# Kernel optimization log

Measured on AMD Instinct MI355X. Metric: run time of the kernel, lower is better.

## Reference

```python
import jax, jax.numpy as jnp
import numpy as np

VOCAB = 50000
EMB = 200        # embedding_size
CAP = 3          # capitalization_size
IN = EMB + CAP   # LSTM input size = 203
HID = 128        # LSTMCell(128)
B = 256
T = 500          # comment_length
NC = 6           # num_classes
DENSE = 64


def _lstm_scan(x_tbi, W, b):
    """x_tbi: [T,B,IN]. W: [IN+HID, 4*HID] (tf gate order i, j, f, o), b: [4*HID].
    Returns h sequence [T,B,HID]. forget_bias=1.0 as in tf.contrib.rnn.LSTMCell."""
    h0 = jnp.zeros((x_tbi.shape[1], HID), x_tbi.dtype)

    def step(carry, x):
        h, c = carry
        gates = jnp.concatenate([x, h], axis=-1) @ W + b   # [B, 4*HID]
        i, j, f, o = jnp.split(gates, 4, axis=-1)
        c = jax.nn.sigmoid(f + 1.0) * c + jax.nn.sigmoid(i) * jnp.tanh(j)
        h = jax.nn.sigmoid(o) * jnp.tanh(c)
        return (h, c), h

    _, hs = jax.lax.scan(step, (h0, h0), x_tbi)
    return hs


def setup_inputs() -> dict:
    key = jax.random.key(0)
    ks = jax.random.split(key, 12)
    words = jax.random.randint(ks[0], (B, T), 0, VOCAB, dtype=jnp.int32)
    capitals = jax.random.randint(ks[1], (B, T), 0, CAP, dtype=jnp.int32)
    # word embeddings: random trainable table with a trailing zero-padding row
    word_emb = jax.random.normal(ks[2], (VOCAB + 1, EMB), dtype=jnp.float32) * 0.1
    # capitalization embedding: one_hot_embedding_matrix(3) = [eye(3); zeros(1,3)]
    cap_emb = jnp.concatenate([jnp.eye(CAP, dtype=jnp.float32),
                               jnp.zeros((1, CAP), dtype=jnp.float32)], axis=0)
    def glorot(k, shape):
        lim = np.sqrt(6.0 / (shape[0] + shape[1]))
        return jax.random.uniform(k, shape, jnp.float32, -lim, lim)
    W_fw = glorot(ks[3], (IN + HID, 4 * HID))
    b_fw = jnp.zeros((4 * HID,), jnp.float32)
    W_bw = glorot(ks[4], (IN + HID, 4 * HID))
    b_bw = jnp.zeros((4 * HID,), jnp.float32)
    W1 = glorot(ks[5], (2 * HID, DENSE))
    b1 = jnp.zeros((DENSE,), jnp.float32)
    W2 = glorot(ks[6], (DENSE, NC))
    b2 = jnp.zeros((NC,), jnp.float32)
    return {"words": words, "capitals": capitals, "word_emb": word_emb,
            "cap_emb": cap_emb, "W_fw": W_fw, "b_fw": b_fw,
            "W_bw": W_bw, "b_bw": b_bw, "W1": W1, "b1": b1,
            "W2": W2, "b2": b2}


def reference(words, capitals, word_emb, cap_emb, W_fw, b_fw, W_bw, b_bw,
              W1, b1, W2, b2):
    # embedding lookups and concat -> [B, T, 203]
    x = jnp.concatenate([word_emb[words], cap_emb[capitals]], axis=-1)
    x_tbi = jnp.transpose(x, (1, 0, 2))                    # [T, B, IN]
    # forward direction: take output at last timestep
    h_fw_last = _lstm_scan(x_tbi, W_fw, b_fw)[-1]          # [B, HID]
    # backward direction: bidirectional_dynamic_rnn reverses bw outputs back,
    # so outputs[1][:, 0, :] == last state of scan over the reversed sequence
    h_bw_first = _lstm_scan(x_tbi[::-1], W_bw, b_bw)[-1]   # [B, HID]
    rnn_output = jnp.concatenate([h_fw_last, h_bw_first], axis=1)  # [B, 256]
    dense1 = jax.nn.elu(rnn_output @ W1 + b1)              # [B, 64]
    y_hat = jax.nn.sigmoid(dense1 @ W2 + b2)               # [B, NC]
    return y_hat
```

## Files before the change

### kernel.cpp

```cpp
#include <hip/hip_runtime.h>

#define T 500
#define NB 256
#define VROWS 50001
#define EMB 200
#define KPAD 224
#define MPAD 50048

typedef unsigned short u16;
typedef __attribute__((ext_vector_type(8))) __bf16 bf16x8;
typedef __attribute__((ext_vector_type(8))) short short8;
typedef __attribute__((ext_vector_type(4))) float f32x4;
typedef __attribute__((ext_vector_type(4))) u16 u16x4;
typedef __attribute__((ext_vector_type(4))) int i32x4;

__device__ __forceinline__ u16 f2bf(float x) {
  union { float f; unsigned u; } v; v.f = x;
  unsigned r = (v.u + 0x7fffu + ((v.u >> 16) & 1u)) >> 16;
  return (u16)r;
}
__device__ __forceinline__ float bf2f(u16 b) {
  union { unsigned u; float f; } v; v.u = ((unsigned)b) << 16;
  return v.f;
}
__device__ __forceinline__ float rcp_(float x) { return __builtin_amdgcn_rcpf(x); }
__device__ __forceinline__ float sig_(float x) { return rcp_(1.f + __expf(-x)); }
__device__ __forceinline__ float tanh_(float x) { return 1.f - 2.f * rcp_(1.f + __expf(2.f * x)); }

__global__ void prep_kernel(const int* __restrict__ words, const int* __restrict__ caps,
                            const float* __restrict__ word_emb,
                            const float* __restrict__ cap_emb,
                            const float* __restrict__ Wfw, const float* __restrict__ bfw,
                            const float* __restrict__ Wbw, const float* __restrict__ bbw,
                            int* __restrict__ wordsT, int* __restrict__ capsT,
                            float* __restrict__ Cproj, u16* __restrict__ Apad,
                            u16* __restrict__ Bt) {
  const int S0 = NB * T;
  const int S1 = MPAD * (KPAD / 4);
  const int S2 = 2 * 512 * KPAD;
  const int S3 = 2 * 4 * 512;
  int tid = blockIdx.x * blockDim.x + threadIdx.x;
  int nthr = gridDim.x * blockDim.x;
  for (int i = tid; i < S0 + S1 + S2 + S3; i += nthr) {
    if (i < S0) {
      int b = i / T, t = i - b * T;
      wordsT[t * NB + b] = words[i];
      capsT[t * NB + b]  = caps[i];
    } else if (i < S0 + S1) {
      int idx = i - S0;
      int v = idx / (KPAD / 4), q = idx - v * (KPAD / 4);
      int k = q * 4;
      u16x4 o;
      if (v < VROWS && k < EMB) {
        const float* p = word_emb + (size_t)v * EMB + k;
        o[0] = f2bf(p[0]); o[1] = f2bf(p[1]); o[2] = f2bf(p[2]); o[3] = f2bf(p[3]);
      } else {
        o[0] = o[1] = o[2] = o[3] = 0;
      }
      *(u16x4*)(Apad + (size_t)v * KPAD + k) = o;
    } else if (i < S0 + S1 + S2) {
      int idx = i - S0 - S1;
      int d = idx / (512 * KPAD), rem = idx - d * (512 * KPAD);
      int colp = rem / KPAD, k = rem - colp * KPAD;
      const float* W = d ? Wbw : Wfw;
      int g = colp & 3, jj = colp >> 2;
      Bt[idx] = (k < EMB) ? f2bf(W[k * 512 + g * 128 + jj]) : (u16)0;
    } else {
      int idx = i - S0 - S1 - S2;
      int dir = idx >> 11; int c = (idx >> 9) & 3; int colp = idx & 511;
      int j = colp >> 2, g = colp & 3;
      const float* W = dir ? Wbw : Wfw;
      const float* bias = dir ? bbw : bfw;
      float v = bias[g * 128 + j];
      #pragma unroll
      for (int cc = 0; cc < 3; ++cc)
        v += cap_emb[c * 3 + cc] * W[(200 + cc) * 512 + g * 128 + j];
      Cproj[idx] = v;
    }
  }
}

__global__ __launch_bounds__(256) void vproj_kernel(
    const u16* __restrict__ Apad, const u16* __restrict__ Bt,
    u16* __restrict__ Vfw, u16* __restrict__ Vbw) {
  const int mt = blockIdx.x, nt = blockIdx.y, dir = blockIdx.z;
  const u16* __restrict__ B = Bt + (size_t)dir * 512 * KPAD;
  u16* __restrict__ V = dir ? Vbw : Vfw;

  __shared__ u16 Al[2][128 * 32];
  __shared__ u16 Bl[2][128 * 32];

  const int tid = threadIdx.x;
  const int w = tid >> 6, l = tid & 63;
  const int la = l & 15, lb = l >> 4;
  const int m0 = mt * 128, n0 = nt * 128;

  auto stage = [&](int buf, int ks) {
    int k0 = ks * 32;
    #pragma unroll
    for (int h = 0; h < 2; ++h) {
      int c = w * 128 + h * 64 + l;
      int row = c >> 2, kq = c & 3;
      const u16* ga = Apad + (size_t)(m0 + row) * KPAD + k0 + kq * 8;
      __builtin_amdgcn_global_load_lds(
          (const __attribute__((address_space(1))) void*)ga,
          (__attribute__((address_space(3))) void*)&Al[buf][(w * 128 + h * 64) * 8],
          16, 0, 0);
      const u16* gb = B + (size_t)(n0 + row) * KPAD + k0 + kq * 8;
      __builtin_amdgcn_global_load_lds(
          (const __attribute__((address_space(1))) void*)gb,
          (__attribute__((address_space(3))) void*)&Bl[buf][(w * 128 + h * 64) * 8],
          16, 0, 0);
    }
  };

  f32x4 z = {0.f, 0.f, 0.f, 0.f};
  f32x4 acc[4][4] = {{z,z,z,z},{z,z,z,z},{z,z,z,z},{z,z,z,z}};
  const int wr = w >> 1, wc = w & 1;

  stage(0, 0);
  __syncthreads();
  #pragma unroll 1
  for (int ks = 0; ks < 7; ++ks) {
    int cur = ks & 1;
    if (ks < 6) stage(cur ^ 1, ks + 1);
    bf16x8 af[4], bfr[4];
    #pragma unroll
    for (int m = 0; m < 4; ++m)
      af[m] = *(const bf16x8*)&Al[cur][(wr * 64 + m * 16 + la) * 32 + lb * 8];
    #pragma unroll
    for (int n = 0; n < 4; ++n)
      bfr[n] = *(const bf16x8*)&Bl[cur][(wc * 64 + n * 16 + la) * 32 + lb * 8];
    #pragma unroll
    for (int m = 0; m < 4; ++m)
      #pragma unroll
      for (int n = 0; n < 4; ++n)
        acc[m][n] = __builtin_amdgcn_mfma_f32_16x16x32_bf16(af[m], bfr[n], acc[m][n], 0, 0, 0);
    __syncthreads();
  }

  #pragma unroll
  for (int m = 0; m < 4; ++m) {
    #pragma unroll
    for (int n = 0; n < 4; ++n) {
      #pragma unroll
      for (int r = 0; r < 4; ++r) {
        int v = m0 + wr * 64 + m * 16 + lb * 4 + r;
        int colp = n0 + wc * 64 + n * 16 + la;
        V[(size_t)v * 512 + colp] = f2bf(acc[m][n][r]);
      }
    }
  }
}

template <int P>
__device__ __forceinline__ void lstm_step(
    int t, int dir, int b0, int la, int lb, int j,
    const int* __restrict__ wordsT, const int* __restrict__ capsT,
    const u16* __restrict__ V, const float* __restrict__ Cp,
    const bf16x8 (&bfrag)[4][4], u16 (&hbuf)[2][16][136],
    u16x4 (&vw)[4], f32x4 (&cp)[4],
    i32x4& wio, i32x4& cio, u16x4 (&vwo)[4], f32x4 (&cpo)[4],
    i32x4& wis, i32x4& cis, f32x4& cst, f32x4& hl) {
  {
    int ts = t + 2; if (ts > T - 1) ts = T - 1;
    int tt = dir ? (T - 1 - ts) : ts;
    wis = *(const i32x4*)(wordsT + tt * NB + b0 + lb * 4);
    cis = *(const i32x4*)(capsT + tt * NB + b0 + lb * 4);
  }
  #pragma unroll
  for (int r = 0; r < 4; ++r) {
    vwo[r] = *(const u16x4*)(V + (size_t)wio[r] * 512 + j * 4);
    cpo[r] = *(const f32x4*)(Cp + cio[r] * 512 + j * 4);
  }

  bf16x8 afr[4];
  #pragma unroll
  for (int kk = 0; kk < 4; ++kk)
    afr[kk] = *(const bf16x8*)&hbuf[P][la][kk * 32 + lb * 8];

  f32x4 acc0, acc1, acc2, acc3;
  #pragma unroll
  for (int r = 0; r < 4; ++r) {
    acc0[r] = bf2f(vw[r][0]) + cp[r][0];
    acc1[r] = bf2f(vw[r][1]) + cp[r][1];
    acc2[r] = bf2f(vw[r][2]) + cp[r][2];
    acc3[r] = bf2f(vw[r][3]) + cp[r][3];
  }
  #pragma unroll
  for (int kk = 0; kk < 4; ++kk) {
    acc0 = __builtin_amdgcn_mfma_f32_16x16x32_bf16(afr[kk], bfrag[0][kk], acc0, 0, 0, 0);
    acc1 = __builtin_amdgcn_mfma_f32_16x16x32_bf16(afr[kk], bfrag[1][kk], acc1, 0, 0, 0);
    acc2 = __builtin_amdgcn_mfma_f32_16x16x32_bf16(afr[kk], bfrag[2][kk], acc2, 0, 0, 0);
    acc3 = __builtin_amdgcn_mfma_f32_16x16x32_bf16(afr[kk], bfrag[3][kk], acc3, 0, 0, 0);
  }
  #pragma unroll
  for (int r = 0; r < 4; ++r) {
    float fg = sig_(acc2[r] + 1.f);
    float ig = sig_(acc0[r]);
    float tj = tanh_(acc1[r]);
    float cn = fg * cst[r] + ig * tj;
    cst[r] = cn;
    float hn = sig_(acc3[r]) * tanh_(cn);
    hl[r] = hn;
    hbuf[P ^ 1][lb * 4 + r][j] = f2bf(hn);
  }
  asm volatile("s_waitcnt lgkmcnt(0)\n\ts_barrier" ::: "memory");
}

__global__ __launch_bounds__(512, 1) void lstm_kernel(
    const int* __restrict__ wordsT, const int* __restrict__ capsT,
    const u16* __restrict__ Vfw, const u16* __restrict__ Vbw,
    const float* __restrict__ CprojAll, const float* __restrict__ Wfw,
    const float* __restrict__ Wbw, float* __restrict__ rnn) {
  const int dir = blockIdx.x & 1;
  const int chunk = blockIdx.x >> 1;
  const int b0 = chunk * 16;
  const u16* __restrict__ V = dir ? Vbw : Vfw;
  const float* __restrict__ Cp = CprojAll + dir * 4 * 512;
  const float* __restrict__ W = dir ? Wbw : Wfw;

  const int tid = threadIdx.x;
  const int w = tid >> 6, l = tid & 63, la = l & 15, lb = l >> 4;
  const int j = w * 16 + la;

  bf16x8 bfrag[4][4];
  #pragma unroll
  for (int g = 0; g < 4; ++g) {
    #pragma unroll
    for (int kk = 0; kk < 4; ++kk) {
      short8 t8;
      #pragma unroll
      for (int r = 0; r < 8; ++r) {
        int k = kk * 32 + lb * 8 + r;
        t8[r] = (short)f2bf(W[(203 + k) * 512 + g * 128 + j]);
      }
      bfrag[g][kk] = __builtin_bit_cast(bf16x8, t8);
    }
  }

  __shared__ u16 hbuf[2][16][136];
  for (int i = tid; i < 2 * 16 * 136; i += 512) ((u16*)hbuf)[i] = 0;

  f32x4 cst = {0.f, 0.f, 0.f, 0.f};
  f32x4 hl  = {0.f, 0.f, 0.f, 0.f};

  i32x4 wiA, ciA, wiB, ciB;
  u16x4 vwA[4]; f32x4 cpA[4];
  u16x4 vwB[4]; f32x4 cpB[4];
  {
    int tt0 = dir ? (T - 1) : 0;
    wiA = *(const i32x4*)(wordsT + tt0 * NB + b0 + lb * 4);
    ciA = *(const i32x4*)(capsT + tt0 * NB + b0 + lb * 4);
    int tt1 = dir ? (T - 2) : 1;
    wiB = *(const i32x4*)(wordsT + tt1 * NB + b0 + lb * 4);
    ciB = *(const i32x4*)(capsT + tt1 * NB + b0 + lb * 4);
  }
  #pragma unroll
  for (int r = 0; r < 4; ++r) {
    vwA[r] = *(const u16x4*)(V + (size_t)wiA[r] * 512 + j * 4);
    cpA[r] = *(const f32x4*)(Cp + ciA[r] * 512 + j * 4);
  }
  __syncthreads();

  #pragma unroll 1
  for (int tp = 0; tp < T / 2; ++tp) {
    int t0 = 2 * tp;
    lstm_step<0>(t0,     dir, b0, la, lb, j, wordsT, capsT, V, Cp, bfrag, hbuf,
                 vwA, cpA, wiB, ciB, vwB, cpB, wiA, ciA, cst, hl);
    lstm_step<1>(t0 + 1, dir, b0, la, lb, j, wordsT, capsT, V, Cp, bfrag, hbuf,
                 vwB, cpB, wiA, ciA, vwA, cpA, wiB, ciB, cst, hl);
  }

  #pragma unroll
  for (int r = 0; r < 4; ++r)
    rnn[(size_t)(b0 + lb * 4 + r) * 256 + dir * 128 + j] = hl[r];
}

__global__ void head_kernel(const float* __restrict__ rnn, const float* __restrict__ W1,
                            const float* __restrict__ b1, const float* __restrict__ W2,
                            const float* __restrict__ b2, float* __restrict__ out) {
  int b = blockIdx.x;
  int jj = threadIdx.x;
  __shared__ float d1[64];
  float acc = b1[jj];
  const float* r = rnn + b * 256;
  #pragma unroll 4
  for (int k = 0; k < 256; ++k) acc += r[k] * W1[k * 64 + jj];
  d1[jj] = acc > 0.f ? acc : (__expf(acc) - 1.f);
  __syncthreads();
  if (jj < 6) {
    float a2 = b2[jj];
    #pragma unroll 8
    for (int k = 0; k < 64; ++k) a2 += d1[k] * W2[k * 6 + jj];
    out[b * 6 + jj] = rcp_(1.f + __expf(-a2));
  }
}

extern "C" void kernel_launch(void* const* d_in, const int* in_sizes, int n_in,
                              void* d_out, int out_size, void* d_ws, size_t ws_size,
                              hipStream_t stream) {
  (void)in_sizes; (void)n_in; (void)out_size; (void)ws_size;
  const int*   words    = (const int*)  d_in[0];
  const int*   caps     = (const int*)  d_in[1];
  const float* word_emb = (const float*)d_in[2];
  const float* cap_emb  = (const float*)d_in[3];
  const float* Wfw      = (const float*)d_in[4];
  const float* bfw      = (const float*)d_in[5];
  const float* Wbw      = (const float*)d_in[6];
  const float* bbw      = (const float*)d_in[7];
  const float* W1       = (const float*)d_in[8];
  const float* b1       = (const float*)d_in[9];
  const float* W2       = (const float*)d_in[10];
  const float* b2       = (const float*)d_in[11];
  float* out = (float*)d_out;

  char* base = (char*)d_ws;
  size_t off = 0;
  auto alloc = [&](size_t bytes) {
    char* q = base + off;
    off = (off + bytes + 255) & ~(size_t)255;
    return q;
  };
  u16*   Vfw    = (u16*)  alloc((size_t)MPAD * 512 * 2);
  u16*   Vbw    = (u16*)  alloc((size_t)MPAD * 512 * 2);
  u16*   Apad   = (u16*)  alloc((size_t)MPAD * KPAD * 2);
  u16*   Bt     = (u16*)  alloc((size_t)2 * 512 * KPAD * 2);
  int*   wordsT = (int*)  alloc((size_t)T * NB * 4);
  int*   capsT  = (int*)  alloc((size_t)T * NB * 4);
  float* Cproj  = (float*)alloc((size_t)2 * 4 * 512 * 4);
  float* rnn    = (float*)alloc((size_t)256 * 256 * 4);

  hipLaunchKernelGGL(prep_kernel, dim3(2048), dim3(256), 0, stream,
                     words, caps, word_emb, cap_emb, Wfw, bfw, Wbw, bbw,
                     wordsT, capsT, Cproj, Apad, Bt);
  hipLaunchKernelGGL(vproj_kernel, dim3(MPAD / 128, 4, 2), dim3(256), 0, stream,
                     Apad, Bt, Vfw, Vbw);
  hipLaunchKernelGGL(lstm_kernel, dim3(32), dim3(512), 0, stream,
                     wordsT, capsT, Vfw, Vbw, Cproj, Wfw, Wbw, rnn);
  hipLaunchKernelGGL(head_kernel, dim3(256), dim3(64), 0, stream,
                     rnn, W1, b1, W2, b2, out);
}
```

Before: 670.3 us.

## Deepen LSTM gather prefetch to four steps and XOR-swizzle hidden-state LDS

The recurrent loop now prefetches word indices four steps ahead and gathered input projections two steps ahead, using four rotating register sets so global gather latency has more steps to hide behind the serial recurrence. The padded hidden-state shared buffer is replaced by an unpadded buffer with an XOR swizzle to avoid bank conflicts on reads and writes. The float-to-bf16 conversion now uses the native cast. These changes raise register pressure and add more in-flight loads per step.

```diff
diff --git a/kernel.cpp b/kernel.cpp
--- a/kernel.cpp
+++ b/kernel.cpp
@@ -15,9 +15,8 @@
 typedef __attribute__((ext_vector_type(4))) int i32x4;
 
 __device__ __forceinline__ u16 f2bf(float x) {
-  union { float f; unsigned u; } v; v.f = x;
-  unsigned r = (v.u + 0x7fffu + ((v.u >> 16) & 1u)) >> 16;
-  return (u16)r;
+  __bf16 h = (__bf16)x;
+  return __builtin_bit_cast(u16, h);
 }
 __device__ __forceinline__ float bf2f(u16 b) {
   union { unsigned u; float f; } v; v.u = ((unsigned)b) << 16;
@@ -153,39 +152,43 @@
   }
 }
 
-template <int P>
+template <int PAR>
 __device__ __forceinline__ void lstm_step(
     int t, int dir, int b0, int la, int lb, int j,
     const int* __restrict__ wordsT, const int* __restrict__ capsT,
     const u16* __restrict__ V, const float* __restrict__ Cp,
-    const bf16x8 (&bfrag)[4][4], u16 (&hbuf)[2][16][136],
-    u16x4 (&vw)[4], f32x4 (&cp)[4],
-    i32x4& wio, i32x4& cio, u16x4 (&vwo)[4], f32x4 (&cpo)[4],
-    i32x4& wis, i32x4& cis, f32x4& cst, f32x4& hl) {
+    const bf16x8 (&bfrag)[4][4], u16* __restrict__ hbuf,
+    u16x4 (&vw_c)[4], f32x4 (&cp_c)[4],
+    i32x4& wi_c, i32x4& ci_c,
+    i32x4& wi_g, i32x4& ci_g,
+    u16x4 (&vw_g)[4], f32x4 (&cp_g)[4],
+    f32x4& cst, f32x4& hl) {
   {
-    int ts = t + 2; if (ts > T - 1) ts = T - 1;
+    int ts = t + 4; if (ts > T - 1) ts = T - 1;
     int tt = dir ? (T - 1 - ts) : ts;
-    wis = *(const i32x4*)(wordsT + tt * NB + b0 + lb * 4);
-    cis = *(const i32x4*)(capsT + tt * NB + b0 + lb * 4);
+    wi_c = *(const i32x4*)(wordsT + tt * NB + b0 + lb * 4);
+    ci_c = *(const i32x4*)(capsT + tt * NB + b0 + lb * 4);
   }
   #pragma unroll
   for (int r = 0; r < 4; ++r) {
-    vwo[r] = *(const u16x4*)(V + (size_t)wio[r] * 512 + j * 4);
-    cpo[r] = *(const f32x4*)(Cp + cio[r] * 512 + j * 4);
-  }
-
+    vw_g[r] = *(const u16x4*)(V + (size_t)wi_g[r] * 512 + j * 4);
+    cp_g[r] = *(const f32x4*)(Cp + ci_g[r] * 512 + j * 4);
+  }
+
+  const u16* hb = hbuf + PAR * 2048;
+  const int swz = (la & 7) << 3;
   bf16x8 afr[4];
   #pragma unroll
   for (int kk = 0; kk < 4; ++kk)
-    afr[kk] = *(const bf16x8*)&hbuf[P][la][kk * 32 + lb * 8];
+    afr[kk] = *(const bf16x8*)(hb + ((la * 128 + kk * 32 + lb * 8) ^ swz));
 
   f32x4 acc0, acc1, acc2, acc3;
   #pragma unroll
   for (int r = 0; r < 4; ++r) {
-    acc0[r] = bf2f(vw[r][0]) + cp[r][0];
-    acc1[r] = bf2f(vw[r][1]) + cp[r][1];
-    acc2[r] = bf2f(vw[r][2]) + cp[r][2];
-    acc3[r] = bf2f(vw[r][3]) + cp[r][3];
+    acc0[r] = bf2f(vw_c[r][0]) + cp_c[r][0];
+    acc1[r] = bf2f(vw_c[r][1]) + cp_c[r][1];
+    acc2[r] = bf2f(vw_c[r][2]) + cp_c[r][2];
+    acc3[r] = bf2f(vw_c[r][3]) + cp_c[r][3];
   }
   #pragma unroll
   for (int kk = 0; kk < 4; ++kk) {
@@ -194,6 +197,7 @@
     acc2 = __builtin_amdgcn_mfma_f32_16x16x32_bf16(afr[kk], bfrag[2][kk], acc2, 0, 0, 0);
     acc3 = __builtin_amdgcn_mfma_f32_16x16x32_bf16(afr[kk], bfrag[3][kk], acc3, 0, 0, 0);
   }
+  u16* ho = hbuf + (PAR ^ 1) * 2048;
   #pragma unroll
   for (int r = 0; r < 4; ++r) {
     float fg = sig_(acc2[r] + 1.f);
@@ -203,7 +207,8 @@
     cst[r] = cn;
     float hn = sig_(acc3[r]) * tanh_(cn);
     hl[r] = hn;
-    hbuf[P ^ 1][lb * 4 + r][j] = f2bf(hn);
+    int row = lb * 4 + r;
+    ho[(row * 128 + j) ^ ((row & 7) << 3)] = f2bf(hn);
   }
   asm volatile("s_waitcnt lgkmcnt(0)\n\ts_barrier" ::: "memory");
 }
@@ -239,37 +244,49 @@
     }
   }
 
-  __shared__ u16 hbuf[2][16][136];
-  for (int i = tid; i < 2 * 16 * 136; i += 512) ((u16*)hbuf)[i] = 0;
+  __shared__ u16 hbuf[2 * 16 * 128];
+  for (int i = tid; i < 2 * 16 * 128; i += 512) hbuf[i] = 0;
 
   f32x4 cst = {0.f, 0.f, 0.f, 0.f};
   f32x4 hl  = {0.f, 0.f, 0.f, 0.f};
 
-  i32x4 wiA, ciA, wiB, ciB;
-  u16x4 vwA[4]; f32x4 cpA[4];
-  u16x4 vwB[4]; f32x4 cpB[4];
+  i32x4 wiA, ciA, wiB, ciB, wiC, ciC, wiD, ciD;
+  u16x4 vwA[4], vwB[4], vwC[4], vwD[4];
+  f32x4 cpA[4], cpB[4], cpC[4], cpD[4];
   {
-    int tt0 = dir ? (T - 1) : 0;
-    wiA = *(const i32x4*)(wordsT + tt0 * NB + b0 + lb * 4);
-    ciA = *(const i32x4*)(capsT + tt0 * NB + b0 + lb * 4);
-    int tt1 = dir ? (T - 2) : 1;
-    wiB = *(const i32x4*)(wordsT + tt1 * NB + b0 + lb * 4);
-    ciB = *(const i32x4*)(capsT + tt1 * NB + b0 + lb * 4);
+    int t0 = dir ? (T - 1) : 0;
+    int t1 = dir ? (T - 2) : 1;
+    int t2 = dir ? (T - 3) : 2;
+    int t3 = dir ? (T - 4) : 3;
+    wiA = *(const i32x4*)(wordsT + t0 * NB + b0 + lb * 4);
+    ciA = *(const i32x4*)(capsT + t0 * NB + b0 + lb * 4);
+    wiB = *(const i32x4*)(wordsT + t1 * NB + b0 + lb * 4);
+    ciB = *(const i32x4*)(capsT + t1 * NB + b0 + lb * 4);
+    wiC = *(const i32x4*)(wordsT + t2 * NB + b0 + lb * 4);
+    ciC = *(const i32x4*)(capsT + t2 * NB + b0 + lb * 4);
+    wiD = *(const i32x4*)(wordsT + t3 * NB + b0 + lb * 4);
+    ciD = *(const i32x4*)(capsT + t3 * NB + b0 + lb * 4);
   }
   #pragma unroll
   for (int r = 0; r < 4; ++r) {
     vwA[r] = *(const u16x4*)(V + (size_t)wiA[r] * 512 + j * 4);
     cpA[r] = *(const f32x4*)(Cp + ciA[r] * 512 + j * 4);
+    vwB[r] = *(const u16x4*)(V + (size_t)wiB[r] * 512 + j * 4);
+    cpB[r] = *(const f32x4*)(Cp + ciB[r] * 512 + j * 4);
   }
   __syncthreads();
 
   #pragma unroll 1
-  for (int tp = 0; tp < T / 2; ++tp) {
-    int t0 = 2 * tp;
+  for (int tq = 0; tq < T / 4; ++tq) {
+    int t0 = 4 * tq;
     lstm_step<0>(t0,     dir, b0, la, lb, j, wordsT, capsT, V, Cp, bfrag, hbuf,
-                 vwA, cpA, wiB, ciB, vwB, cpB, wiA, ciA, cst, hl);
+                 vwA, cpA, wiA, ciA, wiC, ciC, vwC, cpC, cst, hl);
     lstm_step<1>(t0 + 1, dir, b0, la, lb, j, wordsT, capsT, V, Cp, bfrag, hbuf,
-                 vwB, cpB, wiA, ciA, vwA, cpA, wiB, ciB, cst, hl);
+                 vwB, cpB, wiB, ciB, wiD, ciD, vwD, cpD, cst, hl);
+    lstm_step<0>(t0 + 2, dir, b0, la, lb, j, wordsT, capsT, V, Cp, bfrag, hbuf,
+                 vwC, cpC, wiC, ciC, wiA, ciA, vwA, cpA, cst, hl);
+    lstm_step<1>(t0 + 3, dir, b0, la, lb, j, wordsT, capsT, V, Cp, bfrag, hbuf,
+                 vwD, cpD, wiD, ciD, wiB, ciB, vwB, cpB, cst, hl);
   }
 
   #pragma unroll
```

New measurement: 633.0 us. 1.06x faster.
